# Performance work log

Measured on AMD Instinct MI355X. Metric: run time of the kernel, lower is better.

Reference implementation:

```python
import jax, jax.numpy as jnp
import numpy as np

B, L = 32, 96
N = B * L
E = B * L * L
HID, LAT, EEMB = 128, 64, 32
NLAYERS = 3
LAMBDA_CONTRAST = 0.05


def _sinusoidal(t, dim):
    half = dim // 2
    freqs = jnp.exp(-jnp.log(10000.0) * jnp.arange(half, dtype=jnp.float32) / (half - 1))
    ang = t[:, None] * freqs[None, :]
    return jnp.concatenate([jnp.sin(ang), jnp.cos(ang)], axis=-1)


def _forward(H_0, X_0, H_1, X_1, cond_embedding, t_graph,
             Wi1, bi1, Wi2, bi2, Wi3, bi3, edge_table,
             We1, be1, We2, be2, Wx, Wh1, bh1, Wh2, bh2, Wout, bout,
             edges, chain_ids, generate_mask, lengths, shift):
    n = H_0.shape[0]
    b = lengths.shape[0]
    batch_ids = jnp.repeat(jnp.arange(b), lengths, total_repeat_length=n)
    t = t_graph[batch_ids]                      # (N,)
    mask = generate_mask
    mask_f = mask.astype(jnp.float32)

    # path interpolation
    tH = t[:, None]
    H_t = jnp.where(mask[:, None], (1.0 - tH) * H_0 + tH * H_1, H_1)
    X_t = jnp.where(mask[:, None], (1.0 - tH) * X_0 + tH * X_1, X_1)
    v_H_target = H_1 - H_0
    v_X_target = X_1 - X_0

    # edge types from chain-id masking (irregular gather)
    row, col = edges[0], edges[1]
    edge_types = (chain_ids[row] != chain_ids[col]).astype(jnp.int32)

    # --- velocity net ---
    t_embed = _sinusoidal(t, HID)
    h = jnp.concatenate([H_t, cond_embedding, t_embed], axis=-1)
    h = jax.nn.relu(h @ Wi1 + bi1)
    h = jax.nn.relu(h @ Wi2 + bi2)
    h = h @ Wi3 + bi3                            # (N, HID)
    eemb = edge_table[edge_types]                # (E, EEMB)

    X = X_t
    for l in range(NLAYERS):
        rel = X[row] - X[col]                    # (E, 3)
        d2 = jnp.sum(rel * rel, axis=-1, keepdims=True)
        ef = jnp.concatenate([h[row], h[col], d2, eemb], axis=-1)
        m = jax.nn.silu(ef @ We1[l] + be1[l])
        m = jax.nn.silu(m @ We2[l] + be2[l])     # (E, HID)
        coef = m @ Wx[l]                         # (E, 1)
        X = X + jax.ops.segment_sum(rel * coef, row, num_segments=n)
        agg = jax.ops.segment_sum(m, row, num_segments=n)
        hh = jnp.concatenate([h, agg], axis=-1)
        h = h + jax.nn.silu(hh @ Wh1[l] + bh1[l]) @ Wh2[l] + bh2[l]

    v_X_pred = jnp.where(mask[:, None], X, 0.0)
    v_H_pred = jnp.where(mask[:, None], h @ Wout + bout, 0.0)

    # --- losses ---
    msum = mask_f.sum() + 1e-8
    def masked_mse(pred, tgt):
        return (jnp.sum((pred - tgt) ** 2, axis=-1) * mask_f).sum() / msum
    loss_H_pos = masked_mse(v_H_pred, v_H_target)
    loss_X_pos = masked_mse(v_X_pred, v_X_target)

    # negatives: roll over node dim (matches torch indexing (arange+shift)%N)
    v_H_target_neg = jnp.roll(H_1, -shift, axis=0) - jnp.roll(H_0, -shift, axis=0)
    v_X_target_neg = jnp.roll(X_1, -shift, axis=0) - jnp.roll(X_0, -shift, axis=0)
    loss_H_neg = masked_mse(v_H_pred, v_H_target_neg)
    loss_X_neg = masked_mse(v_X_pred, v_X_target_neg)

    loss_H = loss_H_pos - LAMBDA_CONTRAST * loss_H_neg
    loss_X = loss_X_pos - LAMBDA_CONTRAST * loss_X_neg
    return jnp.stack([loss_H, loss_X, loss_H_pos, loss_X_pos, loss_H_neg, loss_X_neg])


def setup_inputs() -> dict:
    key = jax.random.key(0)
    ks = iter(jax.random.split(key, 40))
    def nrm(shape, fan_in):
        return jax.random.normal(next(ks), shape, dtype=jnp.float32) / np.sqrt(fan_in)

    # all-pairs edges within each graph (uniform lengths)
    idx = np.arange(L)
    rb, cb = np.repeat(idx, L), np.tile(idx, L)
    off = (np.arange(B) * L)[:, None]
    rows = (off + rb[None, :]).reshape(-1)
    cols = (off + cb[None, :]).reshape(-1)
    edges = jnp.asarray(np.stack([rows, cols]).astype(np.int32))

    d_in_mlp = LAT + 2 * HID       # 320
    d_in_e = 2 * HID + 1 + EEMB    # 289
    inp = {
        "H_0": jax.random.normal(next(ks), (N, LAT), dtype=jnp.float32),
        "X_0": jax.random.normal(next(ks), (N, 3), dtype=jnp.float32),
        "H_1": jax.random.normal(next(ks), (N, LAT), dtype=jnp.float32),
        "X_1": jax.random.normal(next(ks), (N, 3), dtype=jnp.float32),
        "cond_embedding": jax.random.normal(next(ks), (N, HID), dtype=jnp.float32),
        "t_graph": jax.random.uniform(next(ks), (B,), dtype=jnp.float32),
        "Wi1": nrm((d_in_mlp, HID), d_in_mlp), "bi1": jnp.zeros((HID,)),
        "Wi2": nrm((HID, HID), HID), "bi2": jnp.zeros((HID,)),
        "Wi3": nrm((HID, HID), HID), "bi3": jnp.zeros((HID,)),
        "edge_table": jax.random.normal(next(ks), (2, EEMB), dtype=jnp.float32),
        "We1": nrm((NLAYERS, d_in_e, HID), d_in_e), "be1": jnp.zeros((NLAYERS, HID)),
        "We2": nrm((NLAYERS, HID, HID), HID), "be2": jnp.zeros((NLAYERS, HID)),
        "Wx": nrm((NLAYERS, HID, 1), HID) * 0.01,
        "Wh1": nrm((NLAYERS, 2 * HID, HID), 2 * HID), "bh1": jnp.zeros((NLAYERS, HID)),
        "Wh2": nrm((NLAYERS, HID, HID), HID), "bh2": jnp.zeros((NLAYERS, HID)),
        "Wout": nrm((HID, LAT), HID), "bout": jnp.zeros((LAT,)),
        "edges": edges,
        "chain_ids": jax.random.randint(next(ks), (N,), 0, 3).astype(jnp.int32),
        "generate_mask": jax.random.bernoulli(next(ks), 0.5, (N,)),
        "lengths": jnp.full((B,), L, dtype=jnp.int32),
        "shift": 7,
    }
    return inp


def reference(H_0, X_0, H_1, X_1, cond_embedding, t_graph,
              Wi1, bi1, Wi2, bi2, Wi3, bi3, edge_table,
              We1, be1, We2, be2, Wx, Wh1, bh1, Wh2, bh2, Wout, bout,
              edges, chain_ids, generate_mask, lengths, shift):
    return _forward(H_0, X_0, H_1, X_1, cond_embedding, t_graph,
                    Wi1, bi1, Wi2, bi2, Wi3, bi3, edge_table,
                    We1, be1, We2, be2, Wx, Wh1, bh1, Wh2, bh2, Wout, bout,
                    edges, chain_ids, generate_mask, lengths, shift)
```

## Files before the change

### kernel.cpp

```cpp
#include <hip/hip_runtime.h>
#include <hip/hip_bf16.h>
#include <math.h>

#define NBATCH 32
#define LSEQ   96
#define NN     3072
#define HID    128
#define LAT    64
#define EEMB   32

#define OFF_H      0
#define OFF_X      (OFF_H   + NN*HID)
#define OFF_PA     (OFF_X   + NN*3)
#define OFF_AGG    (OFF_PA  + NN*HID)
#define OFF_DX     (OFF_AGG + NN*HID)
#define OFF_ET     (OFF_DX  + NN*3)
#define OFF_ACC    (OFF_ET  + 768)
#define OFF_NBID   (OFF_ACC + 8)
#define OFF_CUM    (OFF_NBID + NN)
#define OFF_PBH    (OFF_CUM + 40)
#define OFF_BPE    (OFF_PBH + NN*HID/2)
#define OFF_BAB    (OFF_BPE + 24576)
#define OFF_BH1    (OFF_BAB + 49152)
#define OFF_BH2    (OFF_BH1 + 49152)
#define OFF_BWO    (OFF_BH2 + 24576)
#define OFF_BWI1   (OFF_BWO + 4096)
#define OFF_BWI2   (OFF_BWI1 + 20480)
#define OFF_BWI3   (OFF_BWI2 + 8192)

typedef short bf16x8 __attribute__((ext_vector_type(8)));
typedef float f32x4  __attribute__((ext_vector_type(4)));

__device__ __forceinline__ short f2bf(float f) {
    unsigned u = __builtin_bit_cast(unsigned, f);
    unsigned r = (u + 0x7FFFu + ((u >> 16) & 1u)) >> 16;
    return (short)r;
}
__device__ __forceinline__ short2 f2bf2(float a, float b) {
    __hip_bfloat162 h = __float22bfloat162_rn(make_float2(a, b));
    short2 r;
    __builtin_memcpy(&r, &h, sizeof(r));
    return r;
}
__device__ __forceinline__ float bf2f(short s) {
    unsigned u = ((unsigned)(unsigned short)s) << 16;
    return __builtin_bit_cast(float, u);
}
__device__ __forceinline__ float silu(float z) {
    return z * __builtin_amdgcn_rcpf(1.0f + __expf(-z));
}

__global__ void k0a_prep(const float* __restrict__ edge_table,
                         const float* __restrict__ We1,
                         const int* __restrict__ lengths,
                         float* __restrict__ ws) {
    int* cum = (int*)(ws + OFF_CUM);
    int* nb  = (int*)(ws + OFF_NBID);
    float* et = ws + OFF_ET;
    int tid = threadIdx.x;
    if (tid == 0) {
        int s = 0;
        for (int b = 0; b < NBATCH; b++) { cum[b] = s; s += lengths[b]; }
        cum[NBATCH] = s;
    }
    if (tid < 8) ws[OFF_ACC + tid] = 0.0f;
    __syncthreads();
    for (int i = tid; i < NN; i += blockDim.x) {
        int b = NBATCH - 1;
        for (int q = 0; q < NBATCH; q++) { if (i < cum[q + 1]) { b = q; break; } }
        nb[i] = b;
    }
    for (int idx = tid; idx < 3 * 2 * HID; idx += blockDim.x) {
        int c = idx & 127;
        int t = (idx >> 7) & 1;
        int l = idx >> 8;
        const float* w = We1 + (l * 289 + 257) * HID + c;
        const float* e = edge_table + t * EEMB;
        float s = 0.f;
        for (int k = 0; k < EEMB; k++) s += e[k] * w[k * HID];
        et[idx] = s;
    }
}

__global__ void k0b_transpose(const float* __restrict__ We1, const float* __restrict__ We2,
                              const float* __restrict__ Wh1, const float* __restrict__ Wh2,
                              const float* __restrict__ Wout, const float* __restrict__ Wi1,
                              const float* __restrict__ Wi2, const float* __restrict__ Wi3,
                              float* __restrict__ ws) {
    int idx = blockIdx.x * 256 + threadIdx.x;
    short* bpe  = (short*)(ws + OFF_BPE);
    short* bab  = (short*)(ws + OFF_BAB);
    short* bh1  = (short*)(ws + OFF_BH1);
    short* bh2  = (short*)(ws + OFF_BH2);
    short* bwo  = (short*)(ws + OFF_BWO);
    short* bwi1 = (short*)(ws + OFF_BWI1);
    short* bwi2 = (short*)(ws + OFF_BWI2);
    short* bwi3 = (short*)(ws + OFF_BWI3);
    if (idx < 49152) {
        int k = idx & 127, n = (idx >> 7) & 127, l = idx >> 14;
        bpe[idx] = f2bf(We2[(l * 128 + k) * 128 + n]);
    } else if (idx < 147456) {
        int q = idx - 49152;
        int k = q & 127, n = (q >> 7) & 255, l = q >> 15;
        float v = (n < 128) ? We1[(l * 289 + k) * 128 + n]
                            : We1[(l * 289 + 128 + k) * 128 + (n - 128)];
        bab[q] = f2bf(v);
    } else if (idx < 245760) {
        int q = idx - 147456;
        int k = q & 255, n = (q >> 8) & 127, l = q >> 15;
        bh1[q] = f2bf(Wh1[(l * 256 + k) * 128 + n]);
    } else if (idx < 294912) {
        int q = idx - 245760;
        int k = q & 127, n = (q >> 7) & 127, l = q >> 14;
        bh2[q] = f2bf(Wh2[(l * 128 + k) * 128 + n]);
    } else if (idx < 303104) {
        int q = idx - 294912;
        int k = q & 127, n = q >> 7;
        bwo[q] = f2bf(Wout[k * 64 + n]);
    } else if (idx < 344064) {
        int q = idx - 303104;
        int n = q / 320, k = q - n * 320;
        bwi1[q] = f2bf(Wi1[k * 128 + n]);
    } else if (idx < 360448) {
        int q = idx - 344064;
        int k = q & 127, n = q >> 7;
        bwi2[q] = f2bf(Wi2[k * 128 + n]);
    } else if (idx < 376832) {
        int q = idx - 360448;
        int k = q & 127, n = q >> 7;
        bwi3[q] = f2bf(Wi3[k * 128 + n]);
    }
}

__global__ void __launch_bounds__(256)
k1s_node_init(const float* __restrict__ H0, const float* __restrict__ X0,
              const float* __restrict__ H1, const float* __restrict__ X1,
              const float* __restrict__ cond, const float* __restrict__ tg,
              const float* __restrict__ bi1, const float* __restrict__ bi2,
              const float* __restrict__ bi3, const float* __restrict__ be1,
              const int* __restrict__ gmask, float* __restrict__ ws) {
    __shared__ short u1[16 * 136];
    __shared__ short u2[16 * 136];
    int rowbase = blockIdx.x * 96 + blockIdx.y * 16;
    int tid = threadIdx.x;
    int w = tid >> 6, lane = tid & 63;
    int quad = lane >> 4, lp = lane & 15;
    int nodeA = rowbase + lp;
    const int* nb = (const int*)(ws + OFF_NBID);
    float t = tg[nb[nodeA]];
    float u = (gmask[nodeA] != 0) ? t : 1.0f;

    if (tid < 48) {
        int node = rowbase + tid / 3, d = tid % 3;
        float tn = tg[nb[node]];
        float un = (gmask[node] != 0) ? tn : 1.0f;
        ws[OFF_X + (size_t)node * 3 + d] =
            (1.0f - un) * X0[(size_t)node * 3 + d] + un * X1[(size_t)node * 3 + d];
    }

    const short* bwi1 = (const short*)(ws + OFF_BWI1);
    const short* bwi2 = (const short*)(ws + OFF_BWI2);
    const short* bwi3 = (const short*)(ws + OFF_BWI3);
    const short* bab  = (const short*)(ws + OFF_BAB);

    f32x4 acc[2];
    acc[0] = (f32x4){0.f, 0.f, 0.f, 0.f};
    acc[1] = (f32x4){0.f, 0.f, 0.f, 0.f};
    for (int s = 0; s < 10; s++) {
        int kb = s * 32 + quad * 8;
        float z[8];
        if (kb < 64) {
            const float* h0 = H0 + (size_t)nodeA * 64 + kb;
            const float* h1 = H1 + (size_t)nodeA * 64 + kb;
            #pragma unroll
            for (int e = 0; e < 8; e++) z[e] = (1.0f - u) * h0[e] + u * h1[e];
        } else if (kb < 192) {
            const float* cp = cond + (size_t)nodeA * 128 + (kb - 64);
            #pragma unroll
            for (int e = 0; e < 8; e++) z[e] = cp[e];
        } else if (kb < 256) {
            #pragma unroll
            for (int e = 0; e < 8; e++) {
                float c = (float)(kb - 192 + e);
                float fr = __expf(-9.2103403719761836f * c / 63.0f);
                z[e] = __sinf(t * fr);
            }
        } else {
            #pragma unroll
            for (int e = 0; e < 8; e++) {
                float c = (float)(kb - 256 + e);
                float fr = __expf(-9.2103403719761836f * c / 63.0f);
                z[e] = __cosf(t * fr);
            }
        }
        bf16x8 af;
        #pragma unroll
        for (int e = 0; e < 8; e += 2) {
            short2 p = f2bf2(z[e], z[e + 1]);
            af[e] = p.x; af[e + 1] = p.y;
        }
        #pragma unroll
        for (int i = 0; i < 2; i++) {
            int ct = 2 * w + i;
            bf16x8 bf = *(const bf16x8*)(bwi1 + (size_t)(16 * ct + lp) * 320 + kb);
            acc[i] = __builtin_amdgcn_mfma_f32_16x16x32_bf16(af, bf, acc[i], 0, 0, 0);
        }
    }
    #pragma unroll
    for (int i = 0; i < 2; i++) {
        int ch = 16 * (2 * w + i) + lp;
        float bb1 = bi1[ch];
        #pragma unroll
        for (int r = 0; r < 4; r++)
            u1[(quad * 4 + r) * 136 + ch] = f2bf(fmaxf(acc[i][r] + bb1, 0.0f));
    }
    __syncthreads();

    acc[0] = (f32x4){0.f, 0.f, 0.f, 0.f};
    acc[1] = (f32x4){0.f, 0.f, 0.f, 0.f};
    #pragma unroll
    for (int s = 0; s < 4; s++) {
        int kb = s * 32 + quad * 8;
        bf16x8 af = *(const bf16x8*)(u1 + lp * 136 + kb);
        #pragma unroll
        for (int i = 0; i < 2; i++) {
            int ct = 2 * w + i;
            bf16x8 bf = *(const bf16x8*)(bwi2 + (size_t)(16 * ct + lp) * 128 + kb);
            acc[i] = __builtin_amdgcn_mfma_f32_16x16x32_bf16(af, bf, acc[i], 0, 0, 0);
        }
    }
    #pragma unroll
    for (int i = 0; i < 2; i++) {
        int ch = 16 * (2 * w + i) + lp;
        float bb2 = bi2[ch];
        #pragma unroll
        for (int r = 0; r < 4; r++)
            u2[(quad * 4 + r) * 136 + ch] = f2bf(fmaxf(acc[i][r] + bb2, 0.0f));
    }
    __syncthreads();

    acc[0] = (f32x4){0.f, 0.f, 0.f, 0.f};
    acc[1] = (f32x4){0.f, 0.f, 0.f, 0.f};
    #pragma unroll
    for (int s = 0; s < 4; s++) {
        int kb = s * 32 + quad * 8;
        bf16x8 af = *(const bf16x8*)(u2 + lp * 136 + kb);
        #pragma unroll
        for (int i = 0; i < 2; i++) {
            int ct = 2 * w + i;
            bf16x8 bf = *(const bf16x8*)(bwi3 + (size_t)(16 * ct + lp) * 128 + kb);
            acc[i] = __builtin_amdgcn_mfma_f32_16x16x32_bf16(af, bf, acc[i], 0, 0, 0);
        }
    }
    #pragma unroll
    for (int i = 0; i < 2; i++) {
        int ch = 16 * (2 * w + i) + lp;
        float bb3 = bi3[ch];
        #pragma unroll
        for (int r = 0; r < 4; r++) {
            int row = quad * 4 + r;
            float h = acc[i][r] + bb3;
            ws[OFF_H + (size_t)(rowbase + row) * 128 + ch] = h;
            u1[row * 136 + ch] = f2bf(h);
        }
    }
    __syncthreads();

    f32x4 acc4[4];
    #pragma unroll
    for (int i = 0; i < 4; i++) acc4[i] = (f32x4){0.f, 0.f, 0.f, 0.f};
    #pragma unroll
    for (int s = 0; s < 4; s++) {
        int kb = s * 32 + quad * 8;
        bf16x8 af = *(const bf16x8*)(u1 + lp * 136 + kb);
        #pragma unroll
        for (int i = 0; i < 4; i++) {
            int ct4 = 4 * w + i;
            bf16x8 bf = *(const bf16x8*)(bab + (size_t)(16 * ct4 + lp) * 128 + kb);
            acc4[i] = __builtin_amdgcn_mfma_f32_16x16x32_bf16(af, bf, acc4[i], 0, 0, 0);
        }
    }
    short* pbh = (short*)(ws + OFF_PBH);
    #pragma unroll
    for (int i = 0; i < 4; i++) {
        int ct4 = 4 * w + i;
        #pragma unroll
        for (int r = 0; r < 4; r++) {
            int node = rowbase + quad * 4 + r;
            if (ct4 < 8) {
                int ch = 16 * ct4 + lp;
                ws[OFF_PA + (size_t)node * 128 + ch] = acc4[i][r] + be1[ch];
            } else {
                int ch = 16 * (ct4 - 8) + lp;
                pbh[(size_t)node * 128 + ch] = f2bf(acc4[i][r]);
            }
        }
    }
}

#define KG 4
__global__ void __launch_bounds__(384)
k3_edge(const float* __restrict__ We1, const float* __restrict__ Wx,
        const float* __restrict__ be2, const int* __restrict__ chain,
        int l, float* __restrict__ ws) {
    __shared__ short bS[128 * 136];
    __shared__ float pe0S[KG * 128], pe1S[KG * 128];
    __shared__ float d2S[KG * 96];
    __shared__ int   selS[KG * 96];
    __shared__ float xS[96 * 3];
    __shared__ float xT[KG * 3];
    __shared__ float wcS[128], wxS[128], be2S[128];
    __shared__ float aggP[6 * 128];
    __shared__ float coefS[96];

    int tid = threadIdx.x;
    int i0 = blockIdx.x * KG;
    int colbase = (i0 / 96) * 96;
    const float* Xc = ws + OFF_X;

    {
        const short* bpe = (const short*)(ws + OFF_BPE) + (size_t)l * 128 * 128;
        for (int idx = tid; idx < 2048; idx += 384) {
            int row = idx >> 4, c = idx & 15;
            *(bf16x8*)(bS + row * 136 + c * 8) = *(const bf16x8*)(bpe + row * 128 + c * 8);
        }
        if (tid < 288) xS[tid] = Xc[colbase * 3 + tid];
        if (tid < KG * 3) xT[tid] = Xc[(size_t)(i0 + tid / 3) * 3 + tid % 3];
    }
    __syncthreads();

    if (tid < 128) {
        #pragma unroll
        for (int g = 0; g < KG; g++) {
            float pav = ws[OFF_PA + (size_t)(i0 + g) * 128 + tid];
            pe0S[g * 128 + tid] = pav + ws[OFF_ET + l * 256 + tid];
            pe1S[g * 128 + tid] = pav + ws[OFF_ET + l * 256 + 128 + tid];
        }
    } else if (tid < 224) {
        int j = tid - 128;
        int cj = chain[colbase + j];
        #pragma unroll
        for (int g = 0; g < KG; g++) {
            float rx = xT[g * 3 + 0] - xS[j * 3 + 0];
            float ry = xT[g * 3 + 1] - xS[j * 3 + 1];
            float rz = xT[g * 3 + 2] - xS[j * 3 + 2];
            d2S[g * 96 + j]  = rx * rx + ry * ry + rz * rz;
            selS[g * 96 + j] = (chain[i0 + g] != cj) ? 1 : 0;
        }
    } else if (tid < 352) {
        int c = tid - 224;
        wcS[c]  = We1[(l * 289 + 256) * 128 + c];
        wxS[c]  = Wx[l * 128 + c];
        be2S[c] = be2[l * 128 + c];
    }

    int w = tid >> 6, lane = tid & 63;
    int quad = lane >> 4, lp = lane & 15;
    int jA = 16 * w + lp;
    const short* pbrow = (const short*)(ws + OFF_PBH) + (size_t)(colbase + jA) * 128;
    bf16x8 pbv[4];
    #pragma unroll
    for (int s = 0; s < 4; s++) pbv[s] = *(const bf16x8*)(pbrow + s * 32 + quad * 8);
    __syncthreads();

    for (int g = 0; g < KG; g++) {
        float d2j = d2S[g * 96 + jA];
        const float* peB = (selS[g * 96 + jA] ? pe1S : pe0S) + g * 128;

        f32x4 acc[8];
        #pragma unroll
        for (int t = 0; t < 8; t++) acc[t] = (f32x4){0.f, 0.f, 0.f, 0.f};

        #pragma unroll
        for (int s = 0; s < 4; s++) {
            int kb = s * 32 + quad * 8;
            float z[8];
            #pragma unroll
            for (int e = 0; e < 8; e++)
                z[e] = silu(peB[kb + e] + bf2f(pbv[s][e]) + d2j * wcS[kb + e]);
            bf16x8 af;
            #pragma unroll
            for (int e = 0; e < 8; e += 2) {
                short2 p = f2bf2(z[e], z[e + 1]);
                af[e] = p.x; af[e + 1] = p.y;
            }
            #pragma unroll
            for (int t = 0; t < 8; t++) {
                bf16x8 bf = *(const bf16x8*)(bS + (16 * t + lp) * 136 + kb);
                acc[t] = __builtin_amdgcn_mfma_f32_16x16x32_bf16(af, bf, acc[t], 0, 0, 0);
            }
        }

        float cp[4] = {0.f, 0.f, 0.f, 0.f};
        #pragma unroll
        for (int t = 0; t < 8; t++) {
            int ch = 16 * t + lp;
            float bb = be2S[ch];
            float wx = wxS[ch];
            float ag = 0.f;
            #pragma unroll
            for (int r = 0; r < 4; r++) {
                float m2 = silu(acc[t][r] + bb);
                ag += m2;
                cp[r] += m2 * wx;
            }
            ag += __shfl_xor(ag, 16);
            ag += __shfl_xor(ag, 32);
            if (lane < 16) aggP[w * 128 + ch] = ag;
        }
        #pragma unroll
        for (int r = 0; r < 4; r++) {
            float v = cp[r];
            v += __shfl_xor(v, 1);
            v += __shfl_xor(v, 2);
            v += __shfl_xor(v, 4);
            v += __shfl_xor(v, 8);
            if (lp == 0) coefS[16 * w + quad * 4 + r] = v;
        }
        __syncthreads();

        if (tid < 128) {
            float s = 0.f;
            #pragma unroll
            for (int q = 0; q < 6; q++) s += aggP[q * 128 + tid];
            ws[OFF_AGG + (size_t)(i0 + g) * 128 + tid] = s;
        }
        if (w < 3) {
            float v = (xT[g * 3 + w] - xS[lane * 3 + w]) * coefS[lane];
            if (lane < 32) v += (xT[g * 3 + w] - xS[(lane + 64) * 3 + w]) * coefS[lane + 64];
            #pragma unroll
            for (int o = 32; o > 0; o >>= 1) v += __shfl_down(v, o);
            if (lane == 0) ws[OFF_DX + (size_t)(i0 + g) * 3 + w] = v;
        }
        if (g < KG - 1) __syncthreads();
    }
}

__global__ void __launch_bounds__(256)
k4s_node_post(const float* __restrict__ bh1, const float* __restrict__ bh2,
              const float* __restrict__ be1, const float* __restrict__ bout,
              const float* __restrict__ H0, const float* __restrict__ X0,
              const float* __restrict__ H1, const float* __restrict__ X1,
              const int* __restrict__ gmask, const int* __restrict__ shiftp,
              int l, float* __restrict__ ws) {
    __shared__ short uS[16 * 136];
    __shared__ short hS[16 * 136];
    __shared__ float redE[4], redN[4];
    __shared__ float sxp, sxn, scnt;
    int rowbase = blockIdx.x * 96 + blockIdx.y * 16;
    int tid = threadIdx.x;
    int w = tid >> 6, lane = tid & 63;
    int quad = lane >> 4, lp = lane & 15;
    int nodeA = rowbase + lp;
    const short* b1 = (const short*)(ws + OFF_BH1) + (size_t)l * 128 * 256;
    const short* b2 = (const short*)(ws + OFF_BH2) + (size_t)l * 128 * 128;

    if (tid == 0) { sxp = 0.f; sxn = 0.f; scnt = 0.f; }
    if (tid < 48) {
        int node = rowbase + tid / 3, d = tid % 3;
        ws[OFF_X + (size_t)node * 3 + d] += ws[OFF_DX + (size_t)node * 3 + d];
    }

    f32x4 acc[2];
    acc[0] = (f32x4){0.f, 0.f, 0.f, 0.f};
    acc[1] = (f32x4){0.f, 0.f, 0.f, 0.f};
    #pragma unroll
    for (int s = 0; s < 8; s++) {
        int kb = s * 32 + quad * 8;
        const float* src = (kb < 128) ? (ws + OFF_H + (size_t)nodeA * 128 + kb)
                                      : (ws + OFF_AGG + (size_t)nodeA * 128 + (kb - 128));
        bf16x8 af;
        #pragma unroll
        for (int e = 0; e < 8; e += 2) {
            short2 p = f2bf2(src[e], src[e + 1]);
            af[e] = p.x; af[e + 1] = p.y;
        }
        #pragma unroll
        for (int i = 0; i < 2; i++) {
            int ct = 2 * w + i;
            bf16x8 bf = *(const bf16x8*)(b1 + (size_t)(16 * ct + lp) * 256 + kb);
            acc[i] = __builtin_amdgcn_mfma_f32_16x16x32_bf16(af, bf, acc[i], 0, 0, 0);
        }
    }
    #pragma unroll
    for (int i = 0; i < 2; i++) {
        int ch = 16 * (2 * w + i) + lp;
        float bb1 = bh1[l * 128 + ch];
        #pragma unroll
        for (int r = 0; r < 4; r++)
            uS[(quad * 4 + r) * 136 + ch] = f2bf(silu(acc[i][r] + bb1));
    }
    __syncthreads();

    acc[0] = (f32x4){0.f, 0.f, 0.f, 0.f};
    acc[1] = (f32x4){0.f, 0.f, 0.f, 0.f};
    #pragma unroll
    for (int s = 0; s < 4; s++) {
        int kb = s * 32 + quad * 8;
        bf16x8 af = *(const bf16x8*)(uS + lp * 136 + kb);
        #pragma unroll
        for (int i = 0; i < 2; i++) {
            int ct = 2 * w + i;
            bf16x8 bf = *(const bf16x8*)(b2 + (size_t)(16 * ct + lp) * 128 + kb);
            acc[i] = __builtin_amdgcn_mfma_f32_16x16x32_bf16(af, bf, acc[i], 0, 0, 0);
        }
    }
    #pragma unroll
    for (int i = 0; i < 2; i++) {
        int ch = 16 * (2 * w + i) + lp;
        float bb2 = bh2[l * 128 + ch];
        #pragma unroll
        for (int r = 0; r < 4; r++) {
            int row = quad * 4 + r;
            size_t off = OFF_H + (size_t)(rowbase + row) * 128 + ch;
            float h = ws[off] + acc[i][r] + bb2;
            ws[off] = h;
            hS[row * 136 + ch] = f2bf(h);
        }
    }
    __syncthreads();

    if (l < 2) {
        const short* bab = (const short*)(ws + OFF_BAB) + (size_t)(l + 1) * 256 * 128;
        f32x4 acc4[4];
        #pragma unroll
        for (int i = 0; i < 4; i++) acc4[i] = (f32x4){0.f, 0.f, 0.f, 0.f};
        #pragma unroll
        for (int s = 0; s < 4; s++) {
            int kb = s * 32 + quad * 8;
            bf16x8 af = *(const bf16x8*)(hS + lp * 136 + kb);
            #pragma unroll
            for (int i = 0; i < 4; i++) {
                int ct4 = 4 * w + i;
                bf16x8 bf = *(const bf16x8*)(bab + (size_t)(16 * ct4 + lp) * 128 + kb);
                acc4[i] = __builtin_amdgcn_mfma_f32_16x16x32_bf16(af, bf, acc4[i], 0, 0, 0);
            }
        }
        short* pbh = (short*)(ws + OFF_PBH);
        #pragma unroll
        for (int i = 0; i < 4; i++) {
            int ct4 = 4 * w + i;
            #pragma unroll
            for (int r = 0; r < 4; r++) {
                int node = rowbase + quad * 4 + r;
                if (ct4 < 8) {
                    int ch = 16 * ct4 + lp;
                    ws[OFF_PA + (size_t)node * 128 + ch] = acc4[i][r] + be1[(l + 1) * 128 + ch];
                } else {
                    int ch = 16 * (ct4 - 8) + lp;
                    pbh[(size_t)node * 128 + ch] = f2bf(acc4[i][r]);
                }
            }
        }
    } else {
        const short* bwo = (const short*)(ws + OFF_BWO);
        f32x4 accv = (f32x4){0.f, 0.f, 0.f, 0.f};
        #pragma unroll
        for (int s = 0; s < 4; s++) {
            int kb = s * 32 + quad * 8;
            bf16x8 af = *(const bf16x8*)(hS + lp * 136 + kb);
            bf16x8 bf = *(const bf16x8*)(bwo + (size_t)(16 * w + lp) * 128 + kb);
            accv = __builtin_amdgcn_mfma_f32_16x16x32_bf16(af, bf, accv, 0, 0, 0);
        }
        int s = shiftp[0] % NN; if (s < 0) s += NN;
        int col = 16 * w + lp;
        float bo = bout[col];
        float ep = 0.f, en = 0.f;
        #pragma unroll
        for (int r = 0; r < 4; r++) {
            int row = rowbase + quad * 4 + r;
            if (gmask[row] != 0) {
                int ip = row + s; if (ip >= NN) ip -= NN;
                float v  = accv[r] + bo;
                float tp = H1[(size_t)row * 64 + col] - H0[(size_t)row * 64 + col];
                float tn = H1[(size_t)ip * 64 + col]  - H0[(size_t)ip * 64 + col];
                float dp = v - tp, dn = v - tn;
                ep += dp * dp;
                en += dn * dn;
            }
        }
        #pragma unroll
        for (int o = 1; o < 64; o <<= 1) {
            ep += __shfl_xor(ep, o);
            en += __shfl_xor(en, o);
        }
        if (lane == 0) { redE[w] = ep; redN[w] = en; }

        if (tid < 16) {
            int node = rowbase + tid;
            if (gmask[node] != 0) {
                int ip = node + s; if (ip >= NN) ip -= NN;
                float xp = 0.f, xn = 0.f;
                #pragma unroll
                for (int d = 0; d < 3; d++) {
                    float xv  = ws[OFF_X + (size_t)node * 3 + d];
                    float tpx = X1[(size_t)node * 3 + d] - X0[(size_t)node * 3 + d];
                    float tnx = X1[(size_t)ip * 3 + d]   - X0[(size_t)ip * 3 + d];
                    xp += (xv - tpx) * (xv - tpx);
                    xn += (xv - tnx) * (xv - tnx);
                }
                atomicAdd(&sxp, xp);
                atomicAdd(&sxn, xn);
                atomicAdd(&scnt, 1.0f);
            }
        }
        __syncthreads();
        if (tid == 0) {
            float eT = redE[0] + redE[1] + redE[2] + redE[3];
            float nT = redN[0] + redN[1] + redN[2] + redN[3];
            float* acc0 = ws + OFF_ACC;
            atomicAdd(acc0 + 0, eT);
            atomicAdd(acc0 + 2, nT);
            atomicAdd(acc0 + 1, sxp);
            atomicAdd(acc0 + 3, sxn);
            atomicAdd(acc0 + 4, scnt);
        }
    }
}

__global__ void k6_final(const float* __restrict__ ws, float* __restrict__ out) {
    if (threadIdx.x == 0) {
        const float* acc = ws + OFF_ACC;
        float msum = acc[4] + 1e-8f;
        float lhp = acc[0] / msum, lxp = acc[1] / msum;
        float lhn = acc[2] / msum, lxn = acc[3] / msum;
        out[0] = lhp - 0.05f * lhn;
        out[1] = lxp - 0.05f * lxn;
        out[2] = lhp;
        out[3] = lxp;
        out[4] = lhn;
        out[5] = lxn;
    }
}

extern "C" void kernel_launch(void* const* d_in, const int* in_sizes, int n_in,
                              void* d_out, int out_size, void* d_ws, size_t ws_size,
                              hipStream_t stream) {
    (void)in_sizes; (void)n_in; (void)out_size; (void)ws_size;
    const float* H0   = (const float*)d_in[0];
    const float* X0   = (const float*)d_in[1];
    const float* H1   = (const float*)d_in[2];
    const float* X1   = (const float*)d_in[3];
    const float* cond = (const float*)d_in[4];
    const float* tg   = (const float*)d_in[5];
    const float* Wi1  = (const float*)d_in[6];
    const float* bi1  = (const float*)d_in[7];
    const float* Wi2  = (const float*)d_in[8];
    const float* bi2  = (const float*)d_in[9];
    const float* Wi3  = (const float*)d_in[10];
    const float* bi3  = (const float*)d_in[11];
    const float* etab = (const float*)d_in[12];
    const float* We1  = (const float*)d_in[13];
    const float* be1  = (const float*)d_in[14];
    const float* We2  = (const float*)d_in[15];
    const float* be2  = (const float*)d_in[16];
    const float* Wx   = (const float*)d_in[17];
    const float* Wh1  = (const float*)d_in[18];
    const float* bh1  = (const float*)d_in[19];
    const float* Wh2  = (const float*)d_in[20];
    const float* bh2  = (const float*)d_in[21];
    const float* Wout = (const float*)d_in[22];
    const float* bout = (const float*)d_in[23];
    const int* chain   = (const int*)d_in[25];
    const int* gmask   = (const int*)d_in[26];
    const int* lengths = (const int*)d_in[27];
    const int* shiftp  = (const int*)d_in[28];
    float* ws  = (float*)d_ws;
    float* out = (float*)d_out;

    k0a_prep<<<1, 256, 0, stream>>>(etab, We1, lengths, ws);
    k0b_transpose<<<1472, 256, 0, stream>>>(We1, We2, Wh1, Wh2, Wout, Wi1, Wi2, Wi3, ws);
    k1s_node_init<<<dim3(NBATCH, 6), 256, 0, stream>>>(H0, X0, H1, X1, cond, tg,
                                                       bi1, bi2, bi3, be1, gmask, ws);
    for (int l = 0; l < 3; l++) {
        k3_edge<<<NN / KG, 384, 0, stream>>>(We1, Wx, be2, chain, l, ws);
        k4s_node_post<<<dim3(NBATCH, 6), 256, 0, stream>>>(bh1, bh2, be1, bout,
                                                           H0, X0, H1, X1, gmask, shiftp, l, ws);
    }
    k6_final<<<1, 64, 0, stream>>>(ws, out);
}
```

Baseline: 390.5 us.

## Merge prep kernels, fold final reduction, and slim edge kernel shared memory

Merges the two setup kernels into one launch and removes the final tiny kernel: the last block of the final node-post pass, detected with an atomic counter, computes the loss outputs. The edge kernel keeps node features and edge-type terms separate instead of precomputing combined tables, and computes distances and chain tests per lane in registers. The We2 tile is stored in shared memory in MFMA fragment order so B loads are contiguous. This cuts two launches, shared memory and a sync phase, at the cost of an extra add per element and a counter that relies on the k0 zeroing and on the last-layer launch only.

After: 389.7 us. Within noise of the previous version (-0.2%).

```diff
diff --git a/kernel.cpp b/kernel.cpp
--- a/kernel.cpp
+++ b/kernel.cpp
@@ -27,6 +27,7 @@
 #define OFF_BWI1   (OFF_BWO + 4096)
 #define OFF_BWI2   (OFF_BWI1 + 20480)
 #define OFF_BWI3   (OFF_BWI2 + 8192)
+#define OFF_CNT    (OFF_BWI3 + 8192)
 
 typedef short bf16x8 __attribute__((ext_vector_type(8)));
 typedef float f32x4  __attribute__((ext_vector_type(4)));
@@ -50,44 +51,43 @@
     return z * __builtin_amdgcn_rcpf(1.0f + __expf(-z));
 }
 
-__global__ void k0a_prep(const float* __restrict__ edge_table,
-                         const float* __restrict__ We1,
-                         const int* __restrict__ lengths,
-                         float* __restrict__ ws) {
-    int* cum = (int*)(ws + OFF_CUM);
-    int* nb  = (int*)(ws + OFF_NBID);
-    float* et = ws + OFF_ET;
+__global__ void k0_all(const float* __restrict__ edge_table, const float* __restrict__ We1,
+                       const int* __restrict__ lengths, const float* __restrict__ We2,
+                       const float* __restrict__ Wh1, const float* __restrict__ Wh2,
+                       const float* __restrict__ Wout, const float* __restrict__ Wi1,
+                       const float* __restrict__ Wi2, const float* __restrict__ Wi3,
+                       float* __restrict__ ws) {
     int tid = threadIdx.x;
-    if (tid == 0) {
-        int s = 0;
-        for (int b = 0; b < NBATCH; b++) { cum[b] = s; s += lengths[b]; }
-        cum[NBATCH] = s;
-    }
-    if (tid < 8) ws[OFF_ACC + tid] = 0.0f;
-    __syncthreads();
-    for (int i = tid; i < NN; i += blockDim.x) {
-        int b = NBATCH - 1;
-        for (int q = 0; q < NBATCH; q++) { if (i < cum[q + 1]) { b = q; break; } }
-        nb[i] = b;
-    }
-    for (int idx = tid; idx < 3 * 2 * HID; idx += blockDim.x) {
-        int c = idx & 127;
-        int t = (idx >> 7) & 1;
-        int l = idx >> 8;
-        const float* w = We1 + (l * 289 + 257) * HID + c;
-        const float* e = edge_table + t * EEMB;
-        float s = 0.f;
-        for (int k = 0; k < EEMB; k++) s += e[k] * w[k * HID];
-        et[idx] = s;
-    }
-}
-
-__global__ void k0b_transpose(const float* __restrict__ We1, const float* __restrict__ We2,
-                              const float* __restrict__ Wh1, const float* __restrict__ Wh2,
-                              const float* __restrict__ Wout, const float* __restrict__ Wi1,
-                              const float* __restrict__ Wi2, const float* __restrict__ Wi3,
-                              float* __restrict__ ws) {
-    int idx = blockIdx.x * 256 + threadIdx.x;
+    if (blockIdx.x == 1472) {
+        int* cum = (int*)(ws + OFF_CUM);
+        int* nb  = (int*)(ws + OFF_NBID);
+        float* et = ws + OFF_ET;
+        if (tid == 0) {
+            int s = 0;
+            for (int b = 0; b < NBATCH; b++) { cum[b] = s; s += lengths[b]; }
+            cum[NBATCH] = s;
+        }
+        if (tid < 8) ws[OFF_ACC + tid] = 0.0f;
+        if (tid < 128) ((unsigned*)(ws + OFF_CNT))[tid] = 0u;
+        __syncthreads();
+        for (int i = tid; i < NN; i += blockDim.x) {
+            int b = NBATCH - 1;
+            for (int q = 0; q < NBATCH; q++) { if (i < cum[q + 1]) { b = q; break; } }
+            nb[i] = b;
+        }
+        for (int idx = tid; idx < 3 * 2 * HID; idx += blockDim.x) {
+            int c = idx & 127;
+            int t = (idx >> 7) & 1;
+            int l = idx >> 8;
+            const float* w = We1 + (l * 289 + 257) * HID + c;
+            const float* e = edge_table + t * EEMB;
+            float s = 0.f;
+            for (int k = 0; k < EEMB; k++) s += e[k] * w[k * HID];
+            et[idx] = s;
+        }
+        return;
+    }
+    int idx = blockIdx.x * 256 + tid;
     short* bpe  = (short*)(ws + OFF_BPE);
     short* bab  = (short*)(ws + OFF_BAB);
     short* bh1  = (short*)(ws + OFF_BH1);
@@ -299,19 +299,27 @@
 }
 
 #define KG 4
+#define SMC_BS    0
+#define SMC_AGG   32768
+#define SMC_PA    35840
+#define SMC_ET    37888
+#define SMC_WC    38912
+#define SMC_COEF  39424
+#define SMC_XT    39808
+#define SMC_CI    39856
 __global__ void __launch_bounds__(384)
-k3_edge(const float* __restrict__ We1, const float* __restrict__ Wx,
-        const float* __restrict__ be2, const int* __restrict__ chain,
-        int l, float* __restrict__ ws) {
-    __shared__ short bS[128 * 136];
-    __shared__ float pe0S[KG * 128], pe1S[KG * 128];
-    __shared__ float d2S[KG * 96];
-    __shared__ int   selS[KG * 96];
-    __shared__ float xS[96 * 3];
-    __shared__ float xT[KG * 3];
-    __shared__ float wcS[128], wxS[128], be2S[128];
-    __shared__ float aggP[6 * 128];
-    __shared__ float coefS[96];
+k3c_edge(const float* __restrict__ We1, const float* __restrict__ Wx,
+         const float* __restrict__ be2, const int* __restrict__ chain,
+         int l, float* __restrict__ ws) {
+    __shared__ __align__(16) char smem[39872];
+    short* bS    = (short*)(smem + SMC_BS);
+    float* aggP  = (float*)(smem + SMC_AGG);
+    float* paS   = (float*)(smem + SMC_PA);
+    float* etS   = (float*)(smem + SMC_ET);
+    float* wcS   = (float*)(smem + SMC_WC);
+    float* coefS = (float*)(smem + SMC_COEF);
+    float* xT    = (float*)(smem + SMC_XT);
+    int*   ciS   = (int*)  (smem + SMC_CI);
 
     int tid = threadIdx.x;
     int i0 = blockIdx.x * KG;
@@ -321,37 +329,21 @@
     {
         const short* bpe = (const short*)(ws + OFF_BPE) + (size_t)l * 128 * 128;
         for (int idx = tid; idx < 2048; idx += 384) {
-            int row = idx >> 4, c = idx & 15;
-            *(bf16x8*)(bS + row * 136 + c * 8) = *(const bf16x8*)(bpe + row * 128 + c * 8);
-        }
-        if (tid < 288) xS[tid] = Xc[colbase * 3 + tid];
+            int t = idx >> 8, s = (idx >> 6) & 3, ln = idx & 63;
+            int lq = ln >> 4, lpp = ln & 15;
+            *(bf16x8*)(bS + idx * 8) =
+                *(const bf16x8*)(bpe + (size_t)(16 * t + lpp) * 128 + s * 32 + lq * 8);
+        }
+        if (tid < 128) {
+            #pragma unroll
+            for (int g = 0; g < KG; g++)
+                paS[g * 128 + tid] = ws[OFF_PA + (size_t)(i0 + g) * 128 + tid];
+            etS[tid]       = ws[OFF_ET + l * 256 + tid];
+            etS[128 + tid] = ws[OFF_ET + l * 256 + 128 + tid];
+            wcS[tid]       = We1[(l * 289 + 256) * 128 + tid];
+        }
         if (tid < KG * 3) xT[tid] = Xc[(size_t)(i0 + tid / 3) * 3 + tid % 3];
-    }
-    __syncthreads();
-
-    if (tid < 128) {
-        #pragma unroll
-        for (int g = 0; g < KG; g++) {
-            float pav = ws[OFF_PA + (size_t)(i0 + g) * 128 + tid];
-            pe0S[g * 128 + tid] = pav + ws[OFF_ET + l * 256 + tid];
-            pe1S[g * 128 + tid] = pav + ws[OFF_ET + l * 256 + 128 + tid];
-        }
-    } else if (tid < 224) {
-        int j = tid - 128;
-        int cj = chain[colbase + j];
-        #pragma unroll
-        for (int g = 0; g < KG; g++) {
-            float rx = xT[g * 3 + 0] - xS[j * 3 + 0];
-            float ry = xT[g * 3 + 1] - xS[j * 3 + 1];
-            float rz = xT[g * 3 + 2] - xS[j * 3 + 2];
-            d2S[g * 96 + j]  = rx * rx + ry * ry + rz * rz;
-            selS[g * 96 + j] = (chain[i0 + g] != cj) ? 1 : 0;
-        }
-    } else if (tid < 352) {
-        int c = tid - 224;
-        wcS[c]  = We1[(l * 289 + 256) * 128 + c];
-        wxS[c]  = Wx[l * 128 + c];
-        be2S[c] = be2[l * 128 + c];
+        if (tid < KG) ciS[tid] = chain[i0 + tid];
     }
 
     int w = tid >> 6, lane = tid & 63;
@@ -361,11 +353,31 @@
     bf16x8 pbv[4];
     #pragma unroll
     for (int s = 0; s < 4; s++) pbv[s] = *(const bf16x8*)(pbrow + s * 32 + quad * 8);
+    float xr0 = Xc[(size_t)(colbase + jA) * 3 + 0];
+    float xr1 = Xc[(size_t)(colbase + jA) * 3 + 1];
+    float xr2 = Xc[(size_t)(colbase + jA) * 3 + 2];
+    int cj = chain[colbase + jA];
+    float be2r[8], wxr[8];
+    #pragma unroll
+    for (int t = 0; t < 8; t++) {
+        int ch = 16 * t + lp;
+        be2r[t] = be2[l * 128 + ch];
+        wxr[t]  = Wx[l * 128 + ch];
+    }
+    float ex0 = 0.f, ex1 = 0.f;
+    if (w < 3) {
+        ex0 = Xc[(size_t)(colbase + lane) * 3 + w];
+        if (lane < 32) ex1 = Xc[(size_t)(colbase + lane + 64) * 3 + w];
+    }
     __syncthreads();
 
     for (int g = 0; g < KG; g++) {
-        float d2j = d2S[g * 96 + jA];
-        const float* peB = (selS[g * 96 + jA] ? pe1S : pe0S) + g * 128;
+        float rx = xT[g * 3 + 0] - xr0;
+        float ry = xT[g * 3 + 1] - xr1;
+        float rz = xT[g * 3 + 2] - xr2;
+        float d2j = rx * rx + ry * ry + rz * rz;
+        const float* etP = etS + ((cj != ciS[g]) ? 128 : 0);
+        const float* paP = paS + g * 128;
 
         f32x4 acc[8];
         #pragma unroll
@@ -377,7 +389,7 @@
             float z[8];
             #pragma unroll
             for (int e = 0; e < 8; e++)
-                z[e] = silu(peB[kb + e] + bf2f(pbv[s][e]) + d2j * wcS[kb + e]);
+                z[e] = silu(paP[kb + e] + etP[kb + e] + bf2f(pbv[s][e]) + d2j * wcS[kb + e]);
             bf16x8 af;
             #pragma unroll
             for (int e = 0; e < 8; e += 2) {
@@ -386,7 +398,7 @@
             }
             #pragma unroll
             for (int t = 0; t < 8; t++) {
-                bf16x8 bf = *(const bf16x8*)(bS + (16 * t + lp) * 136 + kb);
+                bf16x8 bf = *(const bf16x8*)(bS + ((t * 4 + s) * 64 + lane) * 8);
                 acc[t] = __builtin_amdgcn_mfma_f32_16x16x32_bf16(af, bf, acc[t], 0, 0, 0);
             }
         }
@@ -394,19 +406,16 @@
         float cp[4] = {0.f, 0.f, 0.f, 0.f};
         #pragma unroll
         for (int t = 0; t < 8; t++) {
-            int ch = 16 * t + lp;
-            float bb = be2S[ch];
-            float wx = wxS[ch];
             float ag = 0.f;
             #pragma unroll
             for (int r = 0; r < 4; r++) {
-                float m2 = silu(acc[t][r] + bb);
+                float m2 = silu(acc[t][r] + be2r[t]);
                 ag += m2;
-                cp[r] += m2 * wx;
+                cp[r] += m2 * wxr[t];
             }
             ag += __shfl_xor(ag, 16);
             ag += __shfl_xor(ag, 32);
-            if (lane < 16) aggP[w * 128 + ch] = ag;
+            if (lane < 16) aggP[w * 128 + 16 * t + lp] = ag;
         }
         #pragma unroll
         for (int r = 0; r < 4; r++) {
@@ -426,13 +435,13 @@
             ws[OFF_AGG + (size_t)(i0 + g) * 128 + tid] = s;
         }
         if (w < 3) {
-            float v = (xT[g * 3 + w] - xS[lane * 3 + w]) * coefS[lane];
-            if (lane < 32) v += (xT[g * 3 + w] - xS[(lane + 64) * 3 + w]) * coefS[lane + 64];
+            float v = (xT[g * 3 + w] - ex0) * coefS[lane];
+            if (lane < 32) v += (xT[g * 3 + w] - ex1) * coefS[lane + 64];
             #pragma unroll
             for (int o = 32; o > 0; o >>= 1) v += __shfl_down(v, o);
             if (lane == 0) ws[OFF_DX + (size_t)(i0 + g) * 3 + w] = v;
         }
-        if (g < KG - 1) __syncthreads();
+        __syncthreads();
     }
 }
 
@@ -442,7 +451,7 @@
               const float* __restrict__ H0, const float* __restrict__ X0,
               const float* __restrict__ H1, const float* __restrict__ X1,
               const int* __restrict__ gmask, const int* __restrict__ shiftp,
-              int l, float* __restrict__ ws) {
+              int l, float* __restrict__ ws, float* __restrict__ out) {
     __shared__ short uS[16 * 136];
     __shared__ short hS[16 * 136];
     __shared__ float redE[4], redN[4];
@@ -614,22 +623,26 @@
             atomicAdd(acc0 + 1, sxp);
             atomicAdd(acc0 + 3, sxn);
             atomicAdd(acc0 + 4, scnt);
-        }
-    }
-}
-
-__global__ void k6_final(const float* __restrict__ ws, float* __restrict__ out) {
-    if (threadIdx.x == 0) {
-        const float* acc = ws + OFF_ACC;
-        float msum = acc[4] + 1e-8f;
-        float lhp = acc[0] / msum, lxp = acc[1] / msum;
-        float lhn = acc[2] / msum, lxn = acc[3] / msum;
-        out[0] = lhp - 0.05f * lhn;
-        out[1] = lxp - 0.05f * lxn;
-        out[2] = lhp;
-        out[3] = lxp;
-        out[4] = lhn;
-        out[5] = lxn;
+            __threadfence();
+            unsigned o2 = atomicAdd((unsigned*)(ws + OFF_CNT) + 96, 1u);
+            if (o2 == 191u) {
+                __threadfence();
+                float a0 = atomicAdd(acc0 + 0, 0.0f);
+                float a1 = atomicAdd(acc0 + 1, 0.0f);
+                float a2 = atomicAdd(acc0 + 2, 0.0f);
+                float a3 = atomicAdd(acc0 + 3, 0.0f);
+                float a4 = atomicAdd(acc0 + 4, 0.0f);
+                float msum = a4 + 1e-8f;
+                float lhp = a0 / msum, lxp = a1 / msum;
+                float lhn = a2 / msum, lxn = a3 / msum;
+                out[0] = lhp - 0.05f * lhn;
+                out[1] = lxp - 0.05f * lxn;
+                out[2] = lhp;
+                out[3] = lxp;
+                out[4] = lhn;
+                out[5] = lxn;
+            }
+        }
     }
 }
 
@@ -668,14 +681,14 @@
     float* ws  = (float*)d_ws;
     float* out = (float*)d_out;
 
-    k0a_prep<<<1, 256, 0, stream>>>(etab, We1, lengths, ws);
-    k0b_transpose<<<1472, 256, 0, stream>>>(We1, We2, Wh1, Wh2, Wout, Wi1, Wi2, Wi3, ws);
+    k0_all<<<1473, 256, 0, stream>>>(etab, We1, lengths, We2, Wh1, Wh2,
+                                     Wout, Wi1, Wi2, Wi3, ws);
     k1s_node_init<<<dim3(NBATCH, 6), 256, 0, stream>>>(H0, X0, H1, X1, cond, tg,
                                                        bi1, bi2, bi3, be1, gmask, ws);
     for (int l = 0; l < 3; l++) {
-        k3_edge<<<NN / KG, 384, 0, stream>>>(We1, Wx, be2, chain, l, ws);
+        k3c_edge<<<NN / KG, 384, 0, stream>>>(We1, Wx, be2, chain, l, ws);
         k4s_node_post<<<dim3(NBATCH, 6), 256, 0, stream>>>(bh1, bh2, be1, bout,
-                                                           H0, X0, H1, X1, gmask, shiftp, l, ws);
-    }
-    k6_final<<<1, 64, 0, stream>>>(ws, out);
-}
+                                                           H0, X0, H1, X1, gmask, shiftp,
+                                                           l, ws, out);
+    }
+}
```
